# Kernel tuning notes

Measured on AMD Instinct MI355X. Metric: run time of the kernel, lower is better.

The kernel has to match this reference:

```python
import jax, jax.numpy as jnp
import numpy as np

G = 160          # voxel grid extent per axis
N = 300000       # active voxels
CIN, COUT = 64, 128
EPS = 1e-4       # BatchNorm eps from module (0.0001)


def _neighbor_table(pos):
    """pos: [N,3] int32 in [0,G). Returns idx [27,N] int32, -1 where no neighbor voxel exists."""
    n = pos.shape[0]
    flat = (pos[:, 0] * G + pos[:, 1]) * G + pos[:, 2]
    grid = jnp.full((G * G * G,), -1, dtype=jnp.int32).at[flat].set(
        jnp.arange(n, dtype=jnp.int32))
    offs = jnp.array([[dx, dy, dz] for dx in (-1, 0, 1)
                      for dy in (-1, 0, 1) for dz in (-1, 0, 1)], dtype=jnp.int32)
    npos = pos[None, :, :] + offs[:, None, :]              # [27,N,3]
    inb = jnp.all((npos >= 0) & (npos < G), axis=-1)       # [27,N]
    nflat = (npos[..., 0] * G + npos[..., 1]) * G + npos[..., 2]
    nflat = jnp.where(inb, nflat, 0)
    return jnp.where(inb, grid[nflat], -1)                 # [27,N]


def _sparse_conv(feat, nbr_idx, W):
    """Submanifold sparse 3x3x3 conv. feat [N,Cin], nbr_idx [27,N], W [27,Cin,Cout]."""
    n = feat.shape[0]
    acc0 = jnp.zeros((n, W.shape[-1]), dtype=feat.dtype)

    def body(acc, xs):
        idx, Wk = xs                                       # [N], [Cin,Cout]
        valid = (idx >= 0)
        g = feat[jnp.maximum(idx, 0)] * valid[:, None].astype(feat.dtype)
        return acc + g @ Wk, None

    out, _ = jax.lax.scan(body, acc0, (nbr_idx, W))
    return out


def _bn(x, gamma, beta, mean, var):
    # eval-mode BatchNorm1d: (x - mean) / sqrt(var + eps) * gamma + beta
    return (x - mean) * jax.lax.rsqrt(var + EPS) * gamma + beta


def setup_inputs() -> dict:
    key = jax.random.key(0)
    ks = jax.random.split(key, 8)
    rng = np.random.default_rng(0)
    flat = rng.choice(G * G * G, size=N, replace=False)
    pos = np.stack(np.unravel_index(flat, (G, G, G)), axis=-1).astype(np.int32)

    feat = jax.random.normal(ks[0], (N, CIN), dtype=jnp.float32)
    lin_w = jax.random.normal(ks[1], (COUT, CIN), dtype=jnp.float32) / np.sqrt(CIN)
    W1 = jax.random.normal(ks[2], (27, CIN, COUT), dtype=jnp.float32) / np.sqrt(27 * CIN)
    W2 = jax.random.normal(ks[3], (27, COUT, COUT), dtype=jnp.float32) / np.sqrt(27 * COUT)
    return {
        "feat": feat,
        "pos": jnp.asarray(pos),
        "lin_w": lin_w,
        "bn1_gamma": jnp.ones((CIN,), jnp.float32),
        "bn1_beta": jnp.zeros((CIN,), jnp.float32),
        "bn1_mean": 0.1 * jax.random.normal(ks[4], (CIN,), dtype=jnp.float32),
        "bn1_var": 0.5 + jax.random.uniform(ks[5], (CIN,), dtype=jnp.float32),
        "W1": W1,
        "bn2_gamma": jnp.ones((COUT,), jnp.float32),
        "bn2_beta": jnp.zeros((COUT,), jnp.float32),
        "bn2_mean": 0.1 * jax.random.normal(ks[6], (COUT,), dtype=jnp.float32),
        "bn2_var": 0.5 + jax.random.uniform(ks[7], (COUT,), dtype=jnp.float32),
        "W2": W2,
    }


def reference(feat, pos, lin_w, bn1_gamma, bn1_beta, bn1_mean, bn1_var, W1,
              bn2_gamma, bn2_beta, bn2_mean, bn2_var, W2):
    nbr_idx = _neighbor_table(pos)                     # [27,N]
    out1 = feat @ lin_w.T                              # NetworkInNetwork skip
    h = jnp.maximum(_bn(feat, bn1_gamma, bn1_beta, bn1_mean, bn1_var), 0.0)  # LeakyReLU(0)==ReLU
    h = _sparse_conv(h, nbr_idx, W1)
    h = jnp.maximum(_bn(h, bn2_gamma, bn2_beta, bn2_mean, bn2_var), 0.0)
    h = _sparse_conv(h, nbr_idx, W2)
    return out1 + h
```

## Files before the change

### kernel.cpp

```cpp
#include <hip/hip_runtime.h>

#define G    160
#define G3   (G*G*G)
#define NV   300000
#define EPS  1e-4f
#define CAP  24576
#define CPAD 32
#define PCAP 655360
#define TOTIDX 896
#define NS1  (27*192)

typedef unsigned short u16;
typedef __attribute__((ext_vector_type(8))) short bf16x8;
typedef __attribute__((ext_vector_type(4))) float f32x4;

#define OFF_PART 0ull
#define OFF_GRID 0ull
#define OFF_PIN  167772160ull
#define OFF_PDST (OFF_PIN  + 2654208ull)
#define OFF_RI   (OFF_PDST + 2654208ull)
#define OFF_PERM (OFF_RI   + 1200000ull)
#define OFF_CNT  (OFF_PERM + 1200000ull)
#define OFF_H0   (OFF_CNT  + 8192ull)
#define OFF_H1   (OFF_H0   + 38400000ull)
#define OFF_W1T  (OFF_H1   + 76800000ull)
#define OFF_W2T  (OFF_W1T  + 442368ull)
#define OFF_LINW (OFF_W2T  + 884736ull)
#define OFF_BNP  (OFF_LINW + 16384ull)
#define WS_NEED  (OFF_BNP  + 1024ull)

__device__ __forceinline__ u16 f2bf(float f) {
  unsigned u = __float_as_uint(f);
  return (u16)((u + 0x7fffu + ((u >> 16) & 1u)) >> 16);
}
__device__ __forceinline__ float bf2f(u16 h) {
  return __uint_as_float(((unsigned)h) << 16);
}

__global__ __launch_bounds__(256) void k_pairs(const int* __restrict__ pos,
                        const int* __restrict__ grid,
                        int* __restrict__ pin, int* __restrict__ pdst,
                        int* __restrict__ rowinfo, int* __restrict__ perm,
                        int* __restrict__ counts) {
  __shared__ int lcnt[27];
  __shared__ int wboff[27][4];
  __shared__ int gbase[27];
  __shared__ int lclass[27];
  __shared__ int coff[27];
  __shared__ int scan[256];
  __shared__ int sgb;
  int t = threadIdx.x, lane = t & 63, wv = t >> 6;
  if (t < 27) { lcnt[t] = 0; lclass[t] = 0; }
  int i = blockIdx.x * 256 + t;
  bool act = (i < NV);
  int p0 = 0, p1 = 1 << 20, p2 = 0;
  if (act) { p0 = pos[3*i]; p1 = pos[3*i+1]; p2 = pos[3*i+2]; }
  __syncthreads();

  int j[26];
  #pragma unroll
  for (int kk = 0; kk < 26; kk++) {
    int k = kk < 13 ? kk : kk + 1;
    int q0 = p0 + k/9 - 1, q1 = p1 + (k/3)%3 - 1, q2 = p2 + k%3 - 1;
    bool inb = (q0 >= 0 && q0 < G && q1 >= 0 && q1 < G && q2 >= 0 && q2 < G);
    int addr = inb ? (q0*G + q1)*G + q2 : 0;
    int jj = grid[addr];
    j[kk] = inb ? jj : -1;
  }

  unsigned vmask = 0;
  #pragma unroll
  for (int kk = 0; kk < 26; kk++) if (j[kk] >= 0) vmask |= 1u << kk;
  int ci = __popc(vmask);

  int myrank = 0;
  if (act) myrank = atomicAdd(&lclass[ci], 1);

  unsigned long long m[26];
  #pragma unroll
  for (int kk = 0; kk < 26; kk++) m[kk] = __ballot(j[kk] >= 0);

  #pragma unroll
  for (int kk = 0; kk < 26; kk++) {
    int k = kk < 13 ? kk : kk + 1;
    if (lane == 0) wboff[k][wv] = atomicAdd(&lcnt[k], (int)__popcll(m[kk]));
  }
  scan[t] = ci;
  __syncthreads();
  #pragma unroll
  for (int d = 1; d < 256; d <<= 1) {
    int val = (t >= d) ? scan[t - d] : 0;
    __syncthreads();
    scan[t] += val;
    __syncthreads();
  }
  if (t < 27 && t != 13)
    gbase[t] = atomicAdd(&counts[t * CPAD], lcnt[t]);
  if (t == 255) sgb = atomicAdd(&counts[TOTIDX], scan[255]);
  if (t == 0) {
    int s = 0;
    #pragma unroll
    for (int c = 0; c < 27; c++) { coff[c] = s; s += lclass[c]; }
  }
  __syncthreads();

  int rbase = sgb + scan[t] - ci;
  int cw = (rbase + ci > PCAP) ? 0 : ci;
  if (act) {
    rowinfo[i] = (rbase << 5) | cw;
    perm[blockIdx.x * 256 + coff[ci] + myrank] = i;
  }

  #pragma unroll
  for (int kk = 0; kk < 26; kk++) {
    if (j[kk] >= 0) {
      int k = kk < 13 ? kk : kk + 1;
      int slot = gbase[k] + wboff[k][wv] + (int)__popcll(m[kk] & ((1ull << lane) - 1ull));
      int dst = rbase + __popc(vmask & ((1u << kk) - 1u));
      if (slot < CAP) {
        pin[k*CAP + slot]  = j[kk];
        pdst[k*CAP + slot] = (dst < PCAP) ? dst : -1;
      }
    }
  }
}

#define NB_BN   18750
#define NB_GRID 1172
__global__ __launch_bounds__(256) void k_prep(const float* __restrict__ feat,
                          const int* __restrict__ pos, int* __restrict__ grid,
                          const float* __restrict__ g1, const float* __restrict__ b1,
                          const float* __restrict__ m1, const float* __restrict__ v1,
                          u16* __restrict__ h0,
                          const float* __restrict__ W1, const float* __restrict__ W2,
                          const float* __restrict__ linw,
                          const float* __restrict__ g2, const float* __restrict__ b2,
                          const float* __restrict__ m2, const float* __restrict__ v2,
                          u16* __restrict__ w1t, u16* __restrict__ w2t,
                          u16* __restrict__ lwt, float* __restrict__ bnp) {
  __shared__ float shf[8192];
  int b = blockIdx.x, t = threadIdx.x;
  if (b < NB_BN) {
    float* ss = shf; float* tt = shf + 64;
    if (t < 64) { float s = g1[t] * rsqrtf(v1[t] + EPS); ss[t] = s; tt[t] = b1[t] - m1[t]*s; }
    __syncthreads();
    long gt = (long)b * 256 + t;
    int c = (int)(gt & 15) * 4;
    float4 x = ((const float4*)feat)[gt];
    ushort4 q;
    q.x = f2bf(fmaxf(x.x*ss[c  ] + tt[c  ], 0.f));
    q.y = f2bf(fmaxf(x.y*ss[c+1] + tt[c+1], 0.f));
    q.z = f2bf(fmaxf(x.z*ss[c+2] + tt[c+2], 0.f));
    q.w = f2bf(fmaxf(x.w*ss[c+3] + tt[c+3], 0.f));
    ((ushort4*)h0)[gt] = q;
  } else if (b < NB_BN + NB_GRID) {
    int i = (b - NB_BN) * 256 + t;
    if (i < NV)
      grid[(pos[3*i] * G + pos[3*i+1]) * G + pos[3*i+2]] = i;
  } else {
    int bb = b - NB_BN - NB_GRID;
    float* tmp = shf;
    if (bb < 27) {
      const float* src = W1 + bb * 8192;
      u16* dst = w1t + bb * 8192;
      for (int u = t; u < 8192; u += 256) tmp[u] = src[u];
      __syncthreads();
      for (int u = t; u < 8192; u += 256) { int c = u >> 6, a = u & 63; dst[c*64 + a] = f2bf(tmp[a*128 + c]); }
    } else if (bb < 54) {
      int k = bb - 27;
      const float* src = W2 + k * 16384;
      u16* dst = w2t + k * 16384;
      for (int h = 0; h < 2; h++) {
        for (int u = t; u < 8192; u += 256) tmp[u] = src[h*8192 + u];
        __syncthreads();
        for (int u = t; u < 8192; u += 256) { int c = u >> 6, a = u & 63; dst[c*128 + h*64 + a] = f2bf(tmp[a*128 + c]); }
        __syncthreads();
      }
    } else if (bb == 54) {
      for (int u = t; u < 8192; u += 256) lwt[u] = f2bf(linw[u]);
    } else {
      if (t < 128) { float s = g2[t] * rsqrtf(v2[t] + EPS); bnp[t] = s; bnp[128 + t] = b2[t] - m2[t]*s; }
    }
  }
}

template<int K, int RS>
__device__ __forceinline__ void stage_rows(const u16* __restrict__ src, const int* sidx, u16* lds) {
  const int LPR = K / 8, RPI = 256 / LPR;
  int t = threadIdx.x, o = t % LPR, r0 = t / LPR;
  #pragma unroll
  for (int r = r0; r < 128; r += RPI) {
    int j = sidx[r];
    int4 val = make_int4(0, 0, 0, 0);
    if (j >= 0) val = *(const int4*)(src + (long)j * RS + o * 8);
    *(int4*)(lds + r * (K + 8) + o * 8) = val;
  }
}

__device__ __forceinline__ void stage_feat(const float* __restrict__ feat, int row0, u16* lds) {
  int t = threadIdx.x, o = t & 15, r0 = t >> 4;
  #pragma unroll
  for (int r = r0; r < 128; r += 16) {
    int row = row0 + r;
    float4 x = make_float4(0.f, 0.f, 0.f, 0.f);
    if (row < NV) x = *(const float4*)(feat + (long)row * 64 + o * 4);
    ushort4 q; q.x = f2bf(x.x); q.y = f2bf(x.y); q.z = f2bf(x.z); q.w = f2bf(x.w);
    *(ushort4*)(lds + r * 72 + o * 4) = q;
  }
}

template<int K>
__device__ __forceinline__ void mma_tile(const u16* As, const u16* __restrict__ wt, f32x4 acc[4][4]) {
  int lane = threadIdx.x & 63, wave = threadIdx.x >> 6;
  int wr = (wave >> 1) * 64, wc = (wave & 1) * 64;
  int lr = lane & 15, lk = (lane >> 4) * 8;
  #pragma unroll
  for (int kk = 0; kk < K; kk += 32) {
    bf16x8 a[4], b[4];
    #pragma unroll
    for (int f = 0; f < 4; f++) a[f] = *(const bf16x8*)(As + (wr + f*16 + lr) * (K + 8) + kk + lk);
    #pragma unroll
    for (int f = 0; f < 4; f++) b[f] = *(const bf16x8*)(wt + (wc + f*16 + lr) * K + kk + lk);
    #pragma unroll
    for (int fr = 0; fr < 4; fr++)
      #pragma unroll
      for (int fc = 0; fc < 4; fc++)
        acc[fr][fc] = __builtin_amdgcn_mfma_f32_16x16x32_bf16(a[fr], b[fc], acc[fr][fc], 0, 0, 0);
  }
}

__device__ __forceinline__ void spill_acc(const f32x4 acc[4][4], u16* As) {
  int t = threadIdx.x, lane = t & 63, wave = t >> 6;
  int wr = (wave >> 1) * 64, wc = (wave & 1) * 64, cr = (lane >> 4) * 4, cc = lane & 15;
  #pragma unroll
  for (int fr = 0; fr < 4; fr++)
    #pragma unroll
    for (int r = 0; r < 4; r++)
      #pragma unroll
      for (int fc = 0; fc < 4; fc++)
        As[(wr + fr*16 + cr + r) * 136 + wc + fc*16 + cc] = f2bf(acc[fr][fc][r]);
}

__global__ __launch_bounds__(256, 4) void k_c1(const u16* __restrict__ h0,
                                               const u16* __restrict__ w1t,
                                               const int* __restrict__ pin,
                                               const int* __restrict__ pdst,
                                               const int* __restrict__ counts,
                                               u16* __restrict__ partial,
                                               u16* __restrict__ h1) {
  __shared__ __align__(16) u16 As[128 * 136];
  __shared__ int sin[128], sdst[128];
  int bx = blockIdx.x, t = threadIdx.x;
  if (bx < NS1) {
    int k = bx / 192, base = (bx % 192) * 128;
    int cnt = counts[k * CPAD]; if (cnt > CAP) cnt = CAP;
    if (base >= cnt) return;
    if (t < 128) sin[t] = (base + t < cnt) ? pin[k*CAP + base + t] : -1;
    else         sdst[t - 128] = (base + t - 128 < cnt) ? pdst[k*CAP + base + t - 128] : -1;
    __syncthreads();
    stage_rows<64, 64>(h0, sin, As);
    __syncthreads();
    f32x4 acc[4][4] = {};
    mma_tile<64>(As, w1t + k * 8192, acc);
    __syncthreads();
    spill_acc(acc, As);
    __syncthreads();
    #pragma unroll
    for (int u = t; u < 2048; u += 256) {
      int r = u >> 4, o = u & 15;
      int d = sdst[r];
      if (d >= 0)
        *(int4*)(partial + (long)d * 128 + o * 8) = *(const int4*)(As + r * 136 + o * 8);
    }
  } else {
    int row0 = (bx - NS1) * 128;
    if (t < 128) sin[t] = (row0 + t < NV) ? row0 + t : -1;
    __syncthreads();
    stage_rows<64, 64>(h0, sin, As);
    __syncthreads();
    f32x4 acc[4][4] = {};
    mma_tile<64>(As, w1t + 13 * 8192, acc);
    __syncthreads();
    spill_acc(acc, As);
    __syncthreads();
    #pragma unroll
    for (int u = t; u < 2048; u += 256) {
      int r = u >> 4, o = u & 15;
      if (row0 + r < NV)
        *(int4*)(h1 + (long)(row0 + r) * 128 + o * 8) = *(const int4*)(As + r * 136 + o * 8);
    }
  }
}

__global__ __launch_bounds__(256, 4) void k_scat2(const u16* __restrict__ h1,
                                                  const u16* __restrict__ w2t,
                                                  const int* __restrict__ pin,
                                                  const int* __restrict__ pdst,
                                                  const int* __restrict__ counts,
                                                  u16* __restrict__ partial) {
  int k = blockIdx.y;
  int cnt = counts[k * CPAD]; if (cnt > CAP) cnt = CAP;
  int base = blockIdx.x * 128;
  if (base >= cnt) return;
  __shared__ __align__(16) u16 As[128 * 136];
  __shared__ int sin[128], sdst[128];
  int t = threadIdx.x;
  if (t < 128) sin[t] = (base + t < cnt) ? pin[k*CAP + base + t] : -1;
  else         sdst[t - 128] = (base + t - 128 < cnt) ? pdst[k*CAP + base + t - 128] : -1;
  __syncthreads();
  stage_rows<128, 128>(h1, sin, As);
  __syncthreads();
  f32x4 acc[4][4] = {};
  mma_tile<128>(As, w2t + k * 16384, acc);
  __syncthreads();
  spill_acc(acc, As);
  __syncthreads();
  #pragma unroll
  for (int u = t; u < 2048; u += 256) {
    int r = u >> 4, o = u & 15;
    int d = sdst[r];
    if (d >= 0)
      *(int4*)(partial + (long)d * 128 + o * 8) = *(const int4*)(As + r * 136 + o * 8);
  }
}

__global__ __launch_bounds__(256, 4) void k_self2(const float* __restrict__ feat,
                                                  const u16* __restrict__ lwt,
                                                  u16* __restrict__ h1,
                                                  const u16* __restrict__ w2t) {
  __shared__ __align__(16) u16 As[128 * 136];
  __shared__ int sidx[128];
  int t = threadIdx.x, row0 = blockIdx.x * 128;
  if (t < 128) sidx[t] = (row0 + t < NV) ? row0 + t : -1;
  __syncthreads();
  f32x4 acc[4][4] = {};
  stage_feat(feat, row0, As);
  __syncthreads();
  mma_tile<64>(As, lwt, acc);
  __syncthreads();
  stage_rows<128, 128>(h1, sidx, As);
  __syncthreads();
  mma_tile<128>(As, w2t + 13 * 16384, acc);
  __syncthreads();
  spill_acc(acc, As);
  __syncthreads();
  #pragma unroll
  for (int u = t; u < 2048; u += 256) {
    int r = u >> 4, o = u & 15;
    if (row0 + r < NV)
      *(int4*)(h1 + (long)(row0 + r) * 128 + o * 8) = *(const int4*)(As + r * 136 + o * 8);
  }
}

__device__ __forceinline__ void gather_csr(int row, int q, int base, int cnt,
                                           const u16* __restrict__ sp,
                                           const u16* __restrict__ partial,
                                           float c[32]) {
  bf16x8 s0[4];
  const u16* srow = sp + (long)row * 128 + q * 32;
  #pragma unroll
  for (int u = 0; u < 4; u++) s0[u] = *(const bf16x8*)(srow + u * 8);
  #pragma unroll
  for (int u = 0; u < 4; u++)
    #pragma unroll
    for (int e = 0; e < 8; e++) c[u*8 + e] = bf2f((u16)s0[u][e]);
  const u16* pr = partial + (long)base * 128 + q * 32;
  int p = 0;
  for (; p + 2 <= cnt; p += 2) {
    bf16x8 a[4], b[4];
    #pragma unroll
    for (int u = 0; u < 4; u++) a[u] = *(const bf16x8*)(pr + u * 8);
    #pragma unroll
    for (int u = 0; u < 4; u++) b[u] = *(const bf16x8*)(pr + 128 + u * 8);
    #pragma unroll
    for (int u = 0; u < 4; u++)
      #pragma unroll
      for (int e = 0; e < 8; e++) c[u*8 + e] += bf2f((u16)a[u][e]) + bf2f((u16)b[u][e]);
    pr += 256;
  }
  if (p < cnt) {
    bf16x8 a[4];
    #pragma unroll
    for (int u = 0; u < 4; u++) a[u] = *(const bf16x8*)(pr + u * 8);
    #pragma unroll
    for (int u = 0; u < 4; u++)
      #pragma unroll
      for (int e = 0; e < 8; e++) c[u*8 + e] += bf2f((u16)a[u][e]);
  }
}

__global__ __launch_bounds__(256) void k_gather1(const int* __restrict__ perm,
                                                 const int* __restrict__ rowinfo,
                                                 const u16* __restrict__ partial,
                                                 const float* __restrict__ bnp,
                                                 u16* __restrict__ h1) {
  long tid = (long)blockIdx.x * 256 + threadIdx.x;
  int idx = (int)(tid >> 2), q = (int)(tid & 3);
  if (idx >= NV) return;
  int row = perm[idx];
  int ri = rowinfo[row];
  int base = (int)((unsigned)ri >> 5), cnt = ri & 31;
  float c[32];
  gather_csr(row, q, base, cnt, h1, partial, c);
  int col0 = q * 32;
  unsigned w[16];
  #pragma unroll
  for (int e = 0; e < 16; e++) {
    float o0 = fmaxf(c[2*e  ] * bnp[col0 + 2*e  ] + bnp[128 + col0 + 2*e  ], 0.f);
    float o1 = fmaxf(c[2*e+1] * bnp[col0 + 2*e+1] + bnp[128 + col0 + 2*e+1], 0.f);
    w[e] = (unsigned)f2bf(o0) | ((unsigned)f2bf(o1) << 16);
  }
  int4* dst = (int4*)(h1 + (long)row * 128 + col0);
  #pragma unroll
  for (int u = 0; u < 4; u++) dst[u] = make_int4(w[4*u], w[4*u+1], w[4*u+2], w[4*u+3]);
}

__global__ __launch_bounds__(256) void k_gather2(const int* __restrict__ perm,
                                                 const int* __restrict__ rowinfo,
                                                 const u16* __restrict__ partial,
                                                 const u16* __restrict__ h1,
                                                 float* __restrict__ out) {
  long tid = (long)blockIdx.x * 256 + threadIdx.x;
  int idx = (int)(tid >> 2), q = (int)(tid & 3);
  if (idx >= NV) return;
  int row = perm[idx];
  int ri = rowinfo[row];
  int base = (int)((unsigned)ri >> 5), cnt = ri & 31;
  float c[32];
  gather_csr(row, q, base, cnt, h1, partial, c);
  float* dst = out + (long)row * 128 + q * 32;
  #pragma unroll
  for (int u = 0; u < 8; u++) {
    f32x4 v;
    #pragma unroll
    for (int e = 0; e < 4; e++) v[e] = c[u*4 + e];
    *(f32x4*)(dst + u * 4) = v;
  }
}

extern "C" void kernel_launch(void* const* d_in, const int* in_sizes, int n_in,
                              void* d_out, int out_size, void* d_ws, size_t ws_size,
                              hipStream_t stream) {
  const float* feat = (const float*)d_in[0];
  const int*   pos  = (const int*)d_in[1];
  const float* linw = (const float*)d_in[2];
  const float* g1 = (const float*)d_in[3], *b1 = (const float*)d_in[4];
  const float* m1 = (const float*)d_in[5], *v1 = (const float*)d_in[6];
  const float* W1 = (const float*)d_in[7];
  const float* g2 = (const float*)d_in[8], *b2 = (const float*)d_in[9];
  const float* m2 = (const float*)d_in[10], *v2 = (const float*)d_in[11];
  const float* W2 = (const float*)d_in[12];

  if (ws_size < WS_NEED) return;

  char* ws = (char*)d_ws;
  u16*   partial = (u16*)(ws + OFF_PART);
  int*   grid    = (int*)(ws + OFF_GRID);
  int*   pin     = (int*)(ws + OFF_PIN);
  int*   pdst    = (int*)(ws + OFF_PDST);
  int*   rowinfo = (int*)(ws + OFF_RI);
  int*   perm    = (int*)(ws + OFF_PERM);
  int*   counts  = (int*)(ws + OFF_CNT);
  u16*   h0      = (u16*)(ws + OFF_H0);
  u16*   h1      = (u16*)(ws + OFF_H1);
  u16*   w1t     = (u16*)(ws + OFF_W1T);
  u16*   w2t     = (u16*)(ws + OFF_W2T);
  u16*   lwt     = (u16*)(ws + OFF_LINW);
  float* bnp     = (float*)(ws + OFF_BNP);
  float* out     = (float*)d_out;

  hipMemsetAsync(grid,  0xFF, (size_t)G3 * 4, stream);
  hipMemsetAsync(counts, 0, 8192, stream);

  k_prep <<<NB_BN + NB_GRID + 56, 256, 0, stream>>>(feat, pos, grid, g1, b1, m1, v1, h0,
                                                    W1, W2, linw, g2, b2, m2, v2,
                                                    w1t, w2t, lwt, bnp);
  k_pairs<<<(NV + 255) / 256, 256, 0, stream>>>(pos, grid, pin, pdst, rowinfo, perm, counts);

  int nself = (NV + 127) / 128;
  dim3 gg(((long)NV * 4 + 255) / 256);
  k_c1     <<<NS1 + nself, 256, 0, stream>>>(h0, w1t, pin, pdst, counts, partial, h1);
  k_gather1<<<gg, 256, 0, stream>>>(perm, rowinfo, partial, bnp, h1);
  k_scat2  <<<dim3(192, 27), 256, 0, stream>>>(h1, w2t, pin, pdst, counts, partial);
  k_self2  <<<nself, 256, 0, stream>>>(feat, lwt, h1, w2t);
  k_gather2<<<gg, 256, 0, stream>>>(perm, rowinfo, partial, h1, out);
}
```

Before: 702.7 us.

## Drop neighbor-count permutation and gather two rows per thread in reduction kernels

Removes the per-block class-sorted permutation built in k_pairs and has each gather thread reduce two rows (idx and idx+NVH) at once instead of one perm-ordered row. The permutation existed to group rows with similar partial counts for less divergence. The dual-row loop is meant to give more independent loads in flight per thread and to drop the perm read and its shared atomics. In exchange, rows are no longer count-sorted, so loop trip counts diverge more, and register use per thread rises.

```diff
diff --git a/kernel.cpp b/kernel.cpp
--- a/kernel.cpp
+++ b/kernel.cpp
@@ -3,6 +3,7 @@
 #define G    160
 #define G3   (G*G*G)
 #define NV   300000
+#define NVH  150000
 #define EPS  1e-4f
 #define CAP  24576
 #define CPAD 32
@@ -19,8 +20,7 @@
 #define OFF_PIN  167772160ull
 #define OFF_PDST (OFF_PIN  + 2654208ull)
 #define OFF_RI   (OFF_PDST + 2654208ull)
-#define OFF_PERM (OFF_RI   + 1200000ull)
-#define OFF_CNT  (OFF_PERM + 1200000ull)
+#define OFF_CNT  (OFF_RI   + 1200000ull)
 #define OFF_H0   (OFF_CNT  + 8192ull)
 #define OFF_H1   (OFF_H0   + 38400000ull)
 #define OFF_W1T  (OFF_H1   + 76800000ull)
@@ -40,17 +40,14 @@
 __global__ __launch_bounds__(256) void k_pairs(const int* __restrict__ pos,
                         const int* __restrict__ grid,
                         int* __restrict__ pin, int* __restrict__ pdst,
-                        int* __restrict__ rowinfo, int* __restrict__ perm,
-                        int* __restrict__ counts) {
+                        int* __restrict__ rowinfo, int* __restrict__ counts) {
   __shared__ int lcnt[27];
   __shared__ int wboff[27][4];
   __shared__ int gbase[27];
-  __shared__ int lclass[27];
-  __shared__ int coff[27];
   __shared__ int scan[256];
   __shared__ int sgb;
   int t = threadIdx.x, lane = t & 63, wv = t >> 6;
-  if (t < 27) { lcnt[t] = 0; lclass[t] = 0; }
+  if (t < 27) lcnt[t] = 0;
   int i = blockIdx.x * 256 + t;
   bool act = (i < NV);
   int p0 = 0, p1 = 1 << 20, p2 = 0;
@@ -73,9 +70,6 @@
   for (int kk = 0; kk < 26; kk++) if (j[kk] >= 0) vmask |= 1u << kk;
   int ci = __popc(vmask);
 
-  int myrank = 0;
-  if (act) myrank = atomicAdd(&lclass[ci], 1);
-
   unsigned long long m[26];
   #pragma unroll
   for (int kk = 0; kk < 26; kk++) m[kk] = __ballot(j[kk] >= 0);
@@ -97,19 +91,11 @@
   if (t < 27 && t != 13)
     gbase[t] = atomicAdd(&counts[t * CPAD], lcnt[t]);
   if (t == 255) sgb = atomicAdd(&counts[TOTIDX], scan[255]);
-  if (t == 0) {
-    int s = 0;
-    #pragma unroll
-    for (int c = 0; c < 27; c++) { coff[c] = s; s += lclass[c]; }
-  }
   __syncthreads();
 
   int rbase = sgb + scan[t] - ci;
   int cw = (rbase + ci > PCAP) ? 0 : ci;
-  if (act) {
-    rowinfo[i] = (rbase << 5) | cw;
-    perm[blockIdx.x * 256 + coff[ci] + myrank] = i;
-  }
+  if (act) rowinfo[i] = (rbase << 5) | cw;
 
   #pragma unroll
   for (int kk = 0; kk < 26; kk++) {
@@ -352,90 +338,114 @@
   }
 }
 
-__device__ __forceinline__ void gather_csr(int row, int q, int base, int cnt,
-                                           const u16* __restrict__ sp,
-                                           const u16* __restrict__ partial,
-                                           float c[32]) {
-  bf16x8 s0[4];
-  const u16* srow = sp + (long)row * 128 + q * 32;
-  #pragma unroll
-  for (int u = 0; u < 4; u++) s0[u] = *(const bf16x8*)(srow + u * 8);
-  #pragma unroll
-  for (int u = 0; u < 4; u++)
-    #pragma unroll
-    for (int e = 0; e < 8; e++) c[u*8 + e] = bf2f((u16)s0[u][e]);
-  const u16* pr = partial + (long)base * 128 + q * 32;
-  int p = 0;
-  for (; p + 2 <= cnt; p += 2) {
+__device__ __forceinline__ void gather_dual(int rowA, int rowB, int q,
+                                            const int* __restrict__ rowinfo,
+                                            const u16* __restrict__ sp,
+                                            const u16* __restrict__ partial,
+                                            float cA[32], float cB[32]) {
+  int riA = rowinfo[rowA], riB = rowinfo[rowB];
+  int baseA = (int)((unsigned)riA >> 5), cntA = riA & 31;
+  int baseB = (int)((unsigned)riB >> 5), cntB = riB & 31;
+  bf16x8 sA[4], sB[4];
+  const u16* srA = sp + (long)rowA * 128 + q * 32;
+  const u16* srB = sp + (long)rowB * 128 + q * 32;
+  #pragma unroll
+  for (int u = 0; u < 4; u++) sA[u] = *(const bf16x8*)(srA + u * 8);
+  #pragma unroll
+  for (int u = 0; u < 4; u++) sB[u] = *(const bf16x8*)(srB + u * 8);
+  #pragma unroll
+  for (int u = 0; u < 4; u++) {
+    #pragma unroll
+    for (int e = 0; e < 8; e++) {
+      cA[u*8 + e] = bf2f((u16)sA[u][e]);
+      cB[u*8 + e] = bf2f((u16)sB[u][e]);
+    }
+  }
+  const u16* prA = partial + (long)baseA * 128 + q * 32;
+  const u16* prB = partial + (long)baseB * 128 + q * 32;
+  int mx = cntA > cntB ? cntA : cntB;
+  for (int p = 0; p < mx; ++p) {
+    bool va = p < cntA, vb = p < cntB;
     bf16x8 a[4], b[4];
-    #pragma unroll
-    for (int u = 0; u < 4; u++) a[u] = *(const bf16x8*)(pr + u * 8);
-    #pragma unroll
-    for (int u = 0; u < 4; u++) b[u] = *(const bf16x8*)(pr + 128 + u * 8);
-    #pragma unroll
-    for (int u = 0; u < 4; u++)
-      #pragma unroll
-      for (int e = 0; e < 8; e++) c[u*8 + e] += bf2f((u16)a[u][e]) + bf2f((u16)b[u][e]);
-    pr += 256;
-  }
-  if (p < cnt) {
-    bf16x8 a[4];
-    #pragma unroll
-    for (int u = 0; u < 4; u++) a[u] = *(const bf16x8*)(pr + u * 8);
-    #pragma unroll
-    for (int u = 0; u < 4; u++)
-      #pragma unroll
-      for (int e = 0; e < 8; e++) c[u*8 + e] += bf2f((u16)a[u][e]);
-  }
-}
-
-__global__ __launch_bounds__(256) void k_gather1(const int* __restrict__ perm,
-                                                 const int* __restrict__ rowinfo,
+    if (va) {
+      #pragma unroll
+      for (int u = 0; u < 4; u++) a[u] = *(const bf16x8*)(prA + u * 8);
+    }
+    if (vb) {
+      #pragma unroll
+      for (int u = 0; u < 4; u++) b[u] = *(const bf16x8*)(prB + u * 8);
+    }
+    if (va) {
+      #pragma unroll
+      for (int u = 0; u < 4; u++) {
+        #pragma unroll
+        for (int e = 0; e < 8; e++) cA[u*8 + e] += bf2f((u16)a[u][e]);
+      }
+    }
+    if (vb) {
+      #pragma unroll
+      for (int u = 0; u < 4; u++) {
+        #pragma unroll
+        for (int e = 0; e < 8; e++) cB[u*8 + e] += bf2f((u16)b[u][e]);
+      }
+    }
+    prA += 128; prB += 128;
+  }
+}
+
+__device__ __forceinline__ void bn_store(u16* __restrict__ h1, int row, int q,
+                                         const float* __restrict__ bnp, const float c[32]) {
+  int col0 = q * 32;
+  unsigned w[16];
+  #pragma unroll
+  for (int e = 0; e < 16; e++) {
+    float o0 = fmaxf(c[2*e  ] * bnp[col0 + 2*e  ] + bnp[128 + col0 + 2*e  ], 0.f);
+    float o1 = fmaxf(c[2*e+1] * bnp[col0 + 2*e+1] + bnp[128 + col0 + 2*e+1], 0.f);
+    w[e] = (unsigned)f2bf(o0) | ((unsigned)f2bf(o1) << 16);
+  }
+  int4* dst = (int4*)(h1 + (long)row * 128 + col0);
+  #pragma unroll
+  for (int u = 0; u < 4; u++) dst[u] = make_int4(w[4*u], w[4*u+1], w[4*u+2], w[4*u+3]);
+}
+
+__device__ __forceinline__ void f32_store(float* __restrict__ out, int row, int q,
+                                          const float c[32]) {
+  float* dst = out + (long)row * 128 + q * 32;
+  #pragma unroll
+  for (int u = 0; u < 8; u++) {
+    f32x4 v;
+    #pragma unroll
+    for (int e = 0; e < 4; e++) v[e] = c[u*4 + e];
+    *(f32x4*)(dst + u * 4) = v;
+  }
+}
+
+__global__ __launch_bounds__(256) void k_gather1(const int* __restrict__ rowinfo,
                                                  const u16* __restrict__ partial,
                                                  const float* __restrict__ bnp,
                                                  u16* __restrict__ h1) {
   long tid = (long)blockIdx.x * 256 + threadIdx.x;
   int idx = (int)(tid >> 2), q = (int)(tid & 3);
-  if (idx >= NV) return;
-  int row = perm[idx];
-  int ri = rowinfo[row];
-  int base = (int)((unsigned)ri >> 5), cnt = ri & 31;
-  float c[32];
-  gather_csr(row, q, base, cnt, h1, partial, c);
-  int col0 = q * 32;
-  unsigned w[16];
-  #pragma unroll
-  for (int e = 0; e < 16; e++) {
-    float o0 = fmaxf(c[2*e  ] * bnp[col0 + 2*e  ] + bnp[128 + col0 + 2*e  ], 0.f);
-    float o1 = fmaxf(c[2*e+1] * bnp[col0 + 2*e+1] + bnp[128 + col0 + 2*e+1], 0.f);
-    w[e] = (unsigned)f2bf(o0) | ((unsigned)f2bf(o1) << 16);
-  }
-  int4* dst = (int4*)(h1 + (long)row * 128 + col0);
-  #pragma unroll
-  for (int u = 0; u < 4; u++) dst[u] = make_int4(w[4*u], w[4*u+1], w[4*u+2], w[4*u+3]);
-}
-
-__global__ __launch_bounds__(256) void k_gather2(const int* __restrict__ perm,
-                                                 const int* __restrict__ rowinfo,
+  if (idx >= NVH) return;
+  int rowA = idx, rowB = idx + NVH;
+  float cA[32], cB[32];
+  gather_dual(rowA, rowB, q, rowinfo, h1, partial, cA, cB);
+  bn_store(h1, rowA, q, bnp, cA);
+  bn_store(h1, rowB, q, bnp, cB);
+}
+
+__global__ __launch_bounds__(256) void k_gather2(const int* __restrict__ rowinfo,
                                                  const u16* __restrict__ partial,
                                                  const u16* __restrict__ h1,
                                                  float* __restrict__ out) {
   long tid = (long)blockIdx.x * 256 + threadIdx.x;
   int idx = (int)(tid >> 2), q = (int)(tid & 3);
-  if (idx >= NV) return;
-  int row = perm[idx];
-  int ri = rowinfo[row];
-  int base = (int)((unsigned)ri >> 5), cnt = ri & 31;
-  float c[32];
-  gather_csr(row, q, base, cnt, h1, partial, c);
-  float* dst = out + (long)row * 128 + q * 32;
-  #pragma unroll
-  for (int u = 0; u < 8; u++) {
-    f32x4 v;
-    #pragma unroll
-    for (int e = 0; e < 4; e++) v[e] = c[u*4 + e];
-    *(f32x4*)(dst + u * 4) = v;
-  }
+  if (idx >= NVH) return;
+  int rowA = idx, rowB = idx + NVH;
+  float cA[32], cB[32];
+  gather_dual(rowA, rowB, q, rowinfo, h1, partial, cA, cB);
+  f32_store(out, rowA, q, cA);
+  f32_store(out, rowB, q, cB);
 }
 
 extern "C" void kernel_launch(void* const* d_in, const int* in_sizes, int n_in,
@@ -459,7 +469,6 @@
   int*   pin     = (int*)(ws + OFF_PIN);
   int*   pdst    = (int*)(ws + OFF_PDST);
   int*   rowinfo = (int*)(ws + OFF_RI);
-  int*   perm    = (int*)(ws + OFF_PERM);
   int*   counts  = (int*)(ws + OFF_CNT);
   u16*   h0      = (u16*)(ws + OFF_H0);
   u16*   h1      = (u16*)(ws + OFF_H1);
@@ -475,13 +484,13 @@
   k_prep <<<NB_BN + NB_GRID + 56, 256, 0, stream>>>(feat, pos, grid, g1, b1, m1, v1, h0,
                                                     W1, W2, linw, g2, b2, m2, v2,
                                                     w1t, w2t, lwt, bnp);
-  k_pairs<<<(NV + 255) / 256, 256, 0, stream>>>(pos, grid, pin, pdst, rowinfo, perm, counts);
+  k_pairs<<<(NV + 255) / 256, 256, 0, stream>>>(pos, grid, pin, pdst, rowinfo, counts);
 
   int nself = (NV + 127) / 128;
-  dim3 gg(((long)NV * 4 + 255) / 256);
+  dim3 gg(((long)NVH * 4 + 255) / 256);
   k_c1     <<<NS1 + nself, 256, 0, stream>>>(h0, w1t, pin, pdst, counts, partial, h1);
-  k_gather1<<<gg, 256, 0, stream>>>(perm, rowinfo, partial, bnp, h1);
+  k_gather1<<<gg, 256, 0, stream>>>(rowinfo, partial, bnp, h1);
   k_scat2  <<<dim3(192, 27), 256, 0, stream>>>(h1, w2t, pin, pdst, counts, partial);
   k_self2  <<<nself, 256, 0, stream>>>(feat, lwt, h1, w2t);
-  k_gather2<<<gg, 256, 0, stream>>>(perm, rowinfo, partial, h1, out);
-}
+  k_gather2<<<gg, 256, 0, stream>>>(rowinfo, partial, h1, out);
+}
```

After: 670.9 us. 1.05x faster.

## Use wave-per-row persistent gather kernels and drop neighbor-count permutation

Applied to the files above, without the earlier changes.

The CSR gather kernels change from four threads per row (32 channels each, rows ordered by a neighbor-count permutation) to one 64-lane wave per row, each lane handling two channels. A fixed grid of 2048 blocks loops over rows in grid-stride fashion and prefetches the next rowinfo. The perm array and its shared-memory class counting in k_pairs are removed, which cuts atomics and a scattered write. Each lane now issues narrow 4-byte loads instead of 16-byte vector loads, and rows with different neighbor counts can run in the same wave.

```diff
diff --git a/kernel.cpp b/kernel.cpp
--- a/kernel.cpp
+++ b/kernel.cpp
@@ -9,6 +9,7 @@
 #define PCAP 655360
 #define TOTIDX 896
 #define NS1  (27*192)
+#define GGB  2048
 
 typedef unsigned short u16;
 typedef __attribute__((ext_vector_type(8))) short bf16x8;
@@ -19,8 +20,7 @@
 #define OFF_PIN  167772160ull
 #define OFF_PDST (OFF_PIN  + 2654208ull)
 #define OFF_RI   (OFF_PDST + 2654208ull)
-#define OFF_PERM (OFF_RI   + 1200000ull)
-#define OFF_CNT  (OFF_PERM + 1200000ull)
+#define OFF_CNT  (OFF_RI   + 1200000ull)
 #define OFF_H0   (OFF_CNT  + 8192ull)
 #define OFF_H1   (OFF_H0   + 38400000ull)
 #define OFF_W1T  (OFF_H1   + 76800000ull)
@@ -40,17 +40,14 @@
 __global__ __launch_bounds__(256) void k_pairs(const int* __restrict__ pos,
                         const int* __restrict__ grid,
                         int* __restrict__ pin, int* __restrict__ pdst,
-                        int* __restrict__ rowinfo, int* __restrict__ perm,
-                        int* __restrict__ counts) {
+                        int* __restrict__ rowinfo, int* __restrict__ counts) {
   __shared__ int lcnt[27];
   __shared__ int wboff[27][4];
   __shared__ int gbase[27];
-  __shared__ int lclass[27];
-  __shared__ int coff[27];
   __shared__ int scan[256];
   __shared__ int sgb;
   int t = threadIdx.x, lane = t & 63, wv = t >> 6;
-  if (t < 27) { lcnt[t] = 0; lclass[t] = 0; }
+  if (t < 27) lcnt[t] = 0;
   int i = blockIdx.x * 256 + t;
   bool act = (i < NV);
   int p0 = 0, p1 = 1 << 20, p2 = 0;
@@ -73,9 +70,6 @@
   for (int kk = 0; kk < 26; kk++) if (j[kk] >= 0) vmask |= 1u << kk;
   int ci = __popc(vmask);
 
-  int myrank = 0;
-  if (act) myrank = atomicAdd(&lclass[ci], 1);
-
   unsigned long long m[26];
   #pragma unroll
   for (int kk = 0; kk < 26; kk++) m[kk] = __ballot(j[kk] >= 0);
@@ -97,19 +91,11 @@
   if (t < 27 && t != 13)
     gbase[t] = atomicAdd(&counts[t * CPAD], lcnt[t]);
   if (t == 255) sgb = atomicAdd(&counts[TOTIDX], scan[255]);
-  if (t == 0) {
-    int s = 0;
-    #pragma unroll
-    for (int c = 0; c < 27; c++) { coff[c] = s; s += lclass[c]; }
-  }
   __syncthreads();
 
   int rbase = sgb + scan[t] - ci;
   int cw = (rbase + ci > PCAP) ? 0 : ci;
-  if (act) {
-    rowinfo[i] = (rbase << 5) | cw;
-    perm[blockIdx.x * 256 + coff[ci] + myrank] = i;
-  }
+  if (act) rowinfo[i] = (rbase << 5) | cw;
 
   #pragma unroll
   for (int kk = 0; kk < 26; kk++) {
@@ -352,89 +338,79 @@
   }
 }
 
-__device__ __forceinline__ void gather_csr(int row, int q, int base, int cnt,
-                                           const u16* __restrict__ sp,
-                                           const u16* __restrict__ partial,
-                                           float c[32]) {
-  bf16x8 s0[4];
-  const u16* srow = sp + (long)row * 128 + q * 32;
-  #pragma unroll
-  for (int u = 0; u < 4; u++) s0[u] = *(const bf16x8*)(srow + u * 8);
-  #pragma unroll
-  for (int u = 0; u < 4; u++)
-    #pragma unroll
-    for (int e = 0; e < 8; e++) c[u*8 + e] = bf2f((u16)s0[u][e]);
-  const u16* pr = partial + (long)base * 128 + q * 32;
-  int p = 0;
-  for (; p + 2 <= cnt; p += 2) {
-    bf16x8 a[4], b[4];
-    #pragma unroll
-    for (int u = 0; u < 4; u++) a[u] = *(const bf16x8*)(pr + u * 8);
-    #pragma unroll
-    for (int u = 0; u < 4; u++) b[u] = *(const bf16x8*)(pr + 128 + u * 8);
-    #pragma unroll
-    for (int u = 0; u < 4; u++)
-      #pragma unroll
-      for (int e = 0; e < 8; e++) c[u*8 + e] += bf2f((u16)a[u][e]) + bf2f((u16)b[u][e]);
-    pr += 256;
-  }
-  if (p < cnt) {
-    bf16x8 a[4];
-    #pragma unroll
-    for (int u = 0; u < 4; u++) a[u] = *(const bf16x8*)(pr + u * 8);
-    #pragma unroll
-    for (int u = 0; u < 4; u++)
-      #pragma unroll
-      for (int e = 0; e < 8; e++) c[u*8 + e] += bf2f((u16)a[u][e]);
-  }
-}
-
-__global__ __launch_bounds__(256) void k_gather1(const int* __restrict__ perm,
-                                                 const int* __restrict__ rowinfo,
+
+__global__ __launch_bounds__(256) void k_gather1(const int* __restrict__ rowinfo,
                                                  const u16* __restrict__ partial,
                                                  const float* __restrict__ bnp,
                                                  u16* __restrict__ h1) {
-  long tid = (long)blockIdx.x * 256 + threadIdx.x;
-  int idx = (int)(tid >> 2), q = (int)(tid & 3);
-  if (idx >= NV) return;
-  int row = perm[idx];
+  int lane = threadIdx.x & 63;
+  int wid  = blockIdx.x * 4 + (threadIdx.x >> 6);
+  int stride = gridDim.x * 4;
+  float s0 = bnp[lane*2], s1 = bnp[lane*2 + 1];
+  float t0 = bnp[128 + lane*2], t1 = bnp[128 + lane*2 + 1];
+  int row = wid;
+  if (row >= NV) return;
   int ri = rowinfo[row];
-  int base = (int)((unsigned)ri >> 5), cnt = ri & 31;
-  float c[32];
-  gather_csr(row, q, base, cnt, h1, partial, c);
-  int col0 = q * 32;
-  unsigned w[16];
-  #pragma unroll
-  for (int e = 0; e < 16; e++) {
-    float o0 = fmaxf(c[2*e  ] * bnp[col0 + 2*e  ] + bnp[128 + col0 + 2*e  ], 0.f);
-    float o1 = fmaxf(c[2*e+1] * bnp[col0 + 2*e+1] + bnp[128 + col0 + 2*e+1], 0.f);
-    w[e] = (unsigned)f2bf(o0) | ((unsigned)f2bf(o1) << 16);
-  }
-  int4* dst = (int4*)(h1 + (long)row * 128 + col0);
-  #pragma unroll
-  for (int u = 0; u < 4; u++) dst[u] = make_int4(w[4*u], w[4*u+1], w[4*u+2], w[4*u+3]);
-}
-
-__global__ __launch_bounds__(256) void k_gather2(const int* __restrict__ perm,
-                                                 const int* __restrict__ rowinfo,
+  while (true) {
+    int nrow = row + stride;
+    int nri = (nrow < NV) ? rowinfo[nrow] : 0;
+    int base = (int)((unsigned)ri >> 5), cnt = ri & 31;
+    unsigned sv = *(const unsigned*)(h1 + (long)row * 128 + lane*2);
+    float c0 = bf2f((u16)(sv & 0xffff)), c1 = bf2f((u16)(sv >> 16));
+    const u16* pr = partial + (long)base * 128 + lane*2;
+    int p = 0;
+    for (; p + 2 <= cnt; p += 2) {
+      unsigned a = *(const unsigned*)pr;
+      unsigned b = *(const unsigned*)(pr + 128);
+      c0 += bf2f((u16)(a & 0xffff)) + bf2f((u16)(b & 0xffff));
+      c1 += bf2f((u16)(a >> 16))    + bf2f((u16)(b >> 16));
+      pr += 256;
+    }
+    if (p < cnt) {
+      unsigned a = *(const unsigned*)pr;
+      c0 += bf2f((u16)(a & 0xffff));
+      c1 += bf2f((u16)(a >> 16));
+    }
+    float o0 = fmaxf(c0 * s0 + t0, 0.f), o1 = fmaxf(c1 * s1 + t1, 0.f);
+    *(unsigned*)(h1 + (long)row * 128 + lane*2) = (unsigned)f2bf(o0) | ((unsigned)f2bf(o1) << 16);
+    if (nrow >= NV) break;
+    row = nrow; ri = nri;
+  }
+}
+
+__global__ __launch_bounds__(256) void k_gather2(const int* __restrict__ rowinfo,
                                                  const u16* __restrict__ partial,
                                                  const u16* __restrict__ h1,
                                                  float* __restrict__ out) {
-  long tid = (long)blockIdx.x * 256 + threadIdx.x;
-  int idx = (int)(tid >> 2), q = (int)(tid & 3);
-  if (idx >= NV) return;
-  int row = perm[idx];
+  int lane = threadIdx.x & 63;
+  int wid  = blockIdx.x * 4 + (threadIdx.x >> 6);
+  int stride = gridDim.x * 4;
+  int row = wid;
+  if (row >= NV) return;
   int ri = rowinfo[row];
-  int base = (int)((unsigned)ri >> 5), cnt = ri & 31;
-  float c[32];
-  gather_csr(row, q, base, cnt, h1, partial, c);
-  float* dst = out + (long)row * 128 + q * 32;
-  #pragma unroll
-  for (int u = 0; u < 8; u++) {
-    f32x4 v;
-    #pragma unroll
-    for (int e = 0; e < 4; e++) v[e] = c[u*4 + e];
-    *(f32x4*)(dst + u * 4) = v;
+  while (true) {
+    int nrow = row + stride;
+    int nri = (nrow < NV) ? rowinfo[nrow] : 0;
+    int base = (int)((unsigned)ri >> 5), cnt = ri & 31;
+    unsigned sv = *(const unsigned*)(h1 + (long)row * 128 + lane*2);
+    float c0 = bf2f((u16)(sv & 0xffff)), c1 = bf2f((u16)(sv >> 16));
+    const u16* pr = partial + (long)base * 128 + lane*2;
+    int p = 0;
+    for (; p + 2 <= cnt; p += 2) {
+      unsigned a = *(const unsigned*)pr;
+      unsigned b = *(const unsigned*)(pr + 128);
+      c0 += bf2f((u16)(a & 0xffff)) + bf2f((u16)(b & 0xffff));
+      c1 += bf2f((u16)(a >> 16))    + bf2f((u16)(b >> 16));
+      pr += 256;
+    }
+    if (p < cnt) {
+      unsigned a = *(const unsigned*)pr;
+      c0 += bf2f((u16)(a & 0xffff));
+      c1 += bf2f((u16)(a >> 16));
+    }
+    *(float2*)(out + (long)row * 128 + lane*2) = make_float2(c0, c1);
+    if (nrow >= NV) break;
+    row = nrow; ri = nri;
   }
 }
 
@@ -459,7 +435,6 @@
   int*   pin     = (int*)(ws + OFF_PIN);
   int*   pdst    = (int*)(ws + OFF_PDST);
   int*   rowinfo = (int*)(ws + OFF_RI);
-  int*   perm    = (int*)(ws + OFF_PERM);
   int*   counts  = (int*)(ws + OFF_CNT);
   u16*   h0      = (u16*)(ws + OFF_H0);
   u16*   h1      = (u16*)(ws + OFF_H1);
@@ -475,13 +450,12 @@
   k_prep <<<NB_BN + NB_GRID + 56, 256, 0, stream>>>(feat, pos, grid, g1, b1, m1, v1, h0,
                                                     W1, W2, linw, g2, b2, m2, v2,
                                                     w1t, w2t, lwt, bnp);
-  k_pairs<<<(NV + 255) / 256, 256, 0, stream>>>(pos, grid, pin, pdst, rowinfo, perm, counts);
+  k_pairs<<<(NV + 255) / 256, 256, 0, stream>>>(pos, grid, pin, pdst, rowinfo, counts);
 
   int nself = (NV + 127) / 128;
-  dim3 gg(((long)NV * 4 + 255) / 256);
   k_c1     <<<NS1 + nself, 256, 0, stream>>>(h0, w1t, pin, pdst, counts, partial, h1);
-  k_gather1<<<gg, 256, 0, stream>>>(perm, rowinfo, partial, bnp, h1);
+  k_gather1<<<GGB, 256, 0, stream>>>(rowinfo, partial, bnp, h1);
   k_scat2  <<<dim3(192, 27), 256, 0, stream>>>(h1, w2t, pin, pdst, counts, partial);
   k_self2  <<<nself, 256, 0, stream>>>(feat, lwt, h1, w2t);
-  k_gather2<<<gg, 256, 0, stream>>>(perm, rowinfo, partial, h1, out);
-}
+  k_gather2<<<GGB, 256, 0, stream>>>(rowinfo, partial, h1, out);
+}
```

Result: faster. 659.4 us (-6.2%).
